# Performance work log

Hardware: AMD Instinct MI355X
Metric: run time of the kernel (lower is better)

## Reference

```python
import jax, jax.numpy as jnp
import numpy as np

NI = 512
HEADS = 8
DH = NI // HEADS  # 64 = attn_chans
EPS = 1e-5

def _ln(x, g, b):
    mu = jnp.mean(x, axis=-1, keepdims=True)
    var = jnp.var(x, axis=-1, keepdims=True)
    return (x - mu) * jax.lax.rsqrt(var + EPS) * g + b

def setup_inputs() -> dict:
    key = jax.random.key(0)
    ks = jax.random.split(key, 5)
    n, c, h, w = 8, NI, 32, 32
    return {
        "x": jax.random.normal(ks[0], (n, c, h, w), jnp.float32),
        "query_x": jax.random.normal(ks[1], (n, c, h, w), jnp.float32),
        "q_ln_g": jnp.ones((c,), jnp.float32),
        "q_ln_b": jnp.zeros((c,), jnp.float32),
        "q_w": jax.random.normal(ks[2], (c, c), jnp.float32) / np.sqrt(c),
        "q_b": jnp.zeros((c,), jnp.float32),
        "kv_ln_g": jnp.ones((c,), jnp.float32),
        "kv_ln_b": jnp.zeros((c,), jnp.float32),
        "kv_w": jax.random.normal(ks[3], (c, 2 * c), jnp.float32) / np.sqrt(c),
        "kv_b": jnp.zeros((2 * c,), jnp.float32),
        "proj_w": jax.random.normal(ks[4], (c, c), jnp.float32) / np.sqrt(c),
        "proj_b": jnp.zeros((c,), jnp.float32),
    }

def reference(x, query_x, q_ln_g, q_ln_b, q_w, q_b, kv_ln_g, kv_ln_b, kv_w, kv_b, proj_w, proj_b):
    n, c, h, w = x.shape
    s = h * w
    xs = x.reshape(n, c, s).transpose(0, 2, 1)        # (n, s, c)
    qx = query_x.reshape(n, c, s).transpose(0, 2, 1)  # (n, s, c)
    q_proj = _ln(qx, q_ln_g, q_ln_b) @ q_w + q_b        # (n, s, c)
    kv = _ln(xs, kv_ln_g, kv_ln_b) @ kv_w + kv_b        # (n, s, 2c)
    cat = jnp.concatenate([q_proj, kv], axis=-1)        # (n, s, 3c)
    # rearrange 'n s (h d3)' with h=HEADS, d3 = 3*DH, then chunk into q,k,v
    cat = cat.reshape(n, s, HEADS, 3 * DH).transpose(0, 2, 1, 3)  # (n, H, s, 3d)
    q, k, v = jnp.split(cat, 3, axis=-1)                # each (n, H, s, d)
    scale = jnp.sqrt(jnp.asarray(DH, q.dtype))          # sqrt(ni/nheads)
    scores = jnp.einsum('nhqd,nhkd->nhqk', q, k) / scale
    attn = jax.nn.softmax(scores, axis=-1)
    o = jnp.einsum('nhqk,nhkd->nhqd', attn, v)          # (n, H, s, d)
    o = o.transpose(0, 2, 1, 3).reshape(n, s, c)        # (n, s, c)
    o = o @ proj_w + proj_b
    return o.transpose(0, 2, 1).reshape(n, c, h, w)
```

## Files before the change

kernel.cpp:

```cpp
#include <hip/hip_runtime.h>
#include <math.h>

namespace {

constexpr int S = 1024;
constexpr int C = 512;
constexpr int NBATCH = 8;
constexpr int RTOT = NBATCH * S;
constexpr int HEADS = 8;
constexpr int DH = 64;

typedef __attribute__((ext_vector_type(8))) short bf16x8;
typedef __attribute__((ext_vector_type(4))) float f32x4;
typedef __attribute__((ext_vector_type(16))) float f32x16;
typedef unsigned short u16;
typedef unsigned int u32;

__device__ __forceinline__ u16 f2bf(float x) {
  union { float f; u32 u; } v; v.f = x;
  u32 r = v.u + 0x7FFF + ((v.u >> 16) & 1);
  return (u16)(r >> 16);
}
__device__ __forceinline__ float bf2f(u16 b) {
  union { u32 u; float f; } v; v.u = (u32)b << 16; return v.f;
}
__device__ __forceinline__ u32 cvtpk(float a, float b) {
  u32 r;
  asm("v_cvt_pk_bf16_f32 %0, %1, %2" : "=v"(r) : "v"(a), "v"(b));
  return r;
}
__device__ __forceinline__ void gl_lds16(const void* g, void* l) {
  auto gp = (const __attribute__((address_space(1))) u32*)g;
  auto lp = (__attribute__((address_space(3))) u32*)l;
  __builtin_amdgcn_global_load_lds(gp, lp, 16, 0, 0);
}

__global__ void ln_fused(const float* __restrict__ x, const float* __restrict__ qx,
                         const float* __restrict__ gx, const float* __restrict__ bx,
                         const float* __restrict__ gq, const float* __restrict__ bq,
                         u16* __restrict__ Xkv, u16* __restrict__ Xq) {
  __shared__ float Ssum[8][32], Ssq[8][32];
  __shared__ float mu_s[32], rs_s[32];
  __shared__ float T[32][65];
  int t = threadIdx.x;
  int si0 = blockIdx.x * 32;
  int isq = blockIdx.y & 1, n = blockIdx.y >> 1;
  const float* in = isq ? qx : x;
  const float* g  = isq ? gq : gx;
  const float* be = isq ? bq : bx;
  u16* out = isq ? Xq : Xkv;

  {
    int sl = t & 31, cg = t >> 5;
    const float* p = in + ((size_t)n * C + cg * 64) * S + si0 + sl;
    float s = 0.f, sq = 0.f;
#pragma unroll 8
    for (int c = 0; c < 64; c++) { float v = p[(size_t)c * S]; s += v; sq += v * v; }
    Ssum[cg][sl] = s; Ssq[cg][sl] = sq;
  }
  __syncthreads();
  if (t < 32) {
    float ss = 0.f, q2 = 0.f;
#pragma unroll
    for (int i = 0; i < 8; i++) { ss += Ssum[i][t]; q2 += Ssq[i][t]; }
    float m = ss * (1.0f / C);
    float var = q2 * (1.0f / C) - m * m;
    mu_s[t] = m; rs_s[t] = rsqrtf(var + 1e-5f);
  }
  __syncthreads();

  int si4 = (t & 7) * 4, cl = t >> 3;
  float4 mu4 = *(const float4*)&mu_s[si4];
  float4 rs4 = *(const float4*)&rs_s[si4];
  int wsl = t >> 3, wc8 = (t & 7) * 8;

  for (int c0 = 0; c0 < C; c0 += 64) {
#pragma unroll
    for (int i = 0; i < 2; i++) {
      int c = c0 + cl + i * 32;
      float4 v = *(const float4*)&in[((size_t)n * C + c) * S + si0 + si4];
      float gg = g[c], bb = be[c];
      T[si4 + 0][cl + i * 32] = (v.x - mu4.x) * rs4.x * gg + bb;
      T[si4 + 1][cl + i * 32] = (v.y - mu4.y) * rs4.y * gg + bb;
      T[si4 + 2][cl + i * 32] = (v.z - mu4.z) * rs4.z * gg + bb;
      T[si4 + 3][cl + i * 32] = (v.w - mu4.w) * rs4.w * gg + bb;
    }
    __syncthreads();
    u16 pk[8];
#pragma unroll
    for (int j = 0; j < 8; j++) pk[j] = f2bf(T[wsl][wc8 + j]);
    *(uint4*)&out[((size_t)(n * S + si0 + wsl)) * C + c0 + wc8] = *(const uint4*)pk;
    __syncthreads();
  }
}

__global__ void prep_w(const float* __restrict__ qw, const float* __restrict__ kvw,
                       const float* __restrict__ pw,
                       u16* __restrict__ Wtq, u16* __restrict__ Wtkv,
                       u16* __restrict__ Wph, u16* __restrict__ Wpl) {
  int z = blockIdx.z;
  int N = (z == 1) ? 1024 : 512;
  int col0 = blockIdx.y * 64;
  if (col0 >= N) return;
  int k0 = blockIdx.x * 64;
  const float* W = (z == 0) ? qw : (z == 1) ? kvw : pw;
  __shared__ float T[64][65];
  int t = threadIdx.x;
  int kl = t >> 4, c4 = (t & 15) * 4;
#pragma unroll
  for (int i = 0; i < 4; i++) {
    float4 v = *(const float4*)&W[(size_t)(k0 + kl + i * 16) * N + col0 + c4];
    T[kl + i * 16][c4 + 0] = v.x; T[kl + i * 16][c4 + 1] = v.y;
    T[kl + i * 16][c4 + 2] = v.z; T[kl + i * 16][c4 + 3] = v.w;
  }
  __syncthreads();
#pragma unroll
  for (int p = 0; p < 2; p++) {
    int cl = (t >> 3) + p * 32, k8 = (t & 7) * 8;
    u16 hi[8], lo[8];
#pragma unroll
    for (int j = 0; j < 8; j++) {
      float f = T[k8 + j][cl];
      u16 hv = f2bf(f);
      hi[j] = hv;
      lo[j] = f2bf(f - bf2f(hv));
    }
    size_t o = (size_t)(col0 + cl) * 512 + k0 + k8;
    if (z == 0) *(uint4*)&Wtq[o] = *(const uint4*)hi;
    else if (z == 1) *(uint4*)&Wtkv[o] = *(const uint4*)hi;
    else { *(uint4*)&Wph[o] = *(const uint4*)hi; *(uint4*)&Wpl[o] = *(const uint4*)lo; }
  }
}

__global__ __launch_bounds__(256, 4) void gemm_qkv(
    const u16* __restrict__ Xq, const u16* __restrict__ Xkv,
    const u16* __restrict__ Wtq, const u16* __restrict__ Wtkv,
    const float* __restrict__ q_b, const float* __restrict__ kv_b,
    u16* __restrict__ Qb, u16* __restrict__ Kb, u16* __restrict__ Vt) {
  __shared__ __attribute__((aligned(16))) u16 As[128 * 64];
  __shared__ __attribute__((aligned(16))) u16 Bs[128 * 64];
  int t = threadIdx.x, wid = t >> 6, lane = t & 63, lr = lane & 15, lg = lane >> 4;
  int colb = blockIdx.x;
  const u16* A; const u16* Wt; const float* bias; int ch0;
  if (colb < 4) { A = Xq;  Wt = Wtq  + (size_t)colb * 128 * 512;       bias = q_b  + colb * 128;       ch0 = colb * 128; }
  else          { A = Xkv; Wt = Wtkv + (size_t)(colb - 4) * 128 * 512; bias = kv_b + (colb - 4) * 128; ch0 = 512 + (colb - 4) * 128; }
  int row0 = blockIdx.y * 128;
  int wr = wid >> 1, wc = wid & 1;
  f32x4 acc[4][4];
#pragma unroll
  for (int m = 0; m < 4; m++)
#pragma unroll
    for (int n = 0; n < 4; n++) acc[m][n] = (f32x4){0.f, 0.f, 0.f, 0.f};

  for (int k0 = 0; k0 < 512; k0 += 64) {
    __syncthreads();
#pragma unroll
    for (int it = 0; it < 4; it++) {
      int chunk = (wid * 4 + it) * 64 + lane;
      int r = chunk >> 3, sg = chunk & 7;
      gl_lds16(A + (size_t)(row0 + r) * 512 + k0 + ((sg ^ (r & 7)) * 8),
               (char*)As + (size_t)chunk * 16);
    }
#pragma unroll
    for (int it = 0; it < 4; it++) {
      int chunk = (wid * 4 + it) * 64 + lane;
      int r = chunk >> 3, sg = chunk & 7;
      gl_lds16(Wt + (size_t)r * 512 + k0 + ((sg ^ (r & 7)) * 8),
               (char*)Bs + (size_t)chunk * 16);
    }
    __syncthreads();
#pragma unroll
    for (int kk = 0; kk < 2; kk++) {
      bf16x8 bfr[4];
#pragma unroll
      for (int n = 0; n < 4; n++) {
        int col = wc * 64 + n * 16 + lr;
        bfr[n] = *(const bf16x8*)((const char*)Bs + col * 128 + (((kk * 4 + lg) ^ (col & 7)) << 4));
      }
#pragma unroll
      for (int m = 0; m < 4; m++) {
        int row = wr * 64 + m * 16 + lr;
        bf16x8 af = *(const bf16x8*)((const char*)As + row * 128 + (((kk * 4 + lg) ^ (row & 7)) << 4));
#pragma unroll
        for (int n = 0; n < 4; n++)
          acc[m][n] = __builtin_amdgcn_mfma_f32_16x16x32_bf16(af, bfr[n], acc[m][n], 0, 0, 0);
      }
    }
  }
#pragma unroll
  for (int m = 0; m < 4; m++)
#pragma unroll
    for (int n = 0; n < 4; n++) {
      int colg = wc * 64 + n * 16 + lr;
      int ch = ch0 + colg;
      int h = ch / 192, role = (ch >> 6) % 3, d = ch & 63;
      float bs = bias[colg];
      float qsc = (role == 0) ? 0.18033688f : 1.0f;
      int growb = row0 + wr * 64 + m * 16 + lg * 4;
      int nn = growb >> 10, ssi0 = growb & (S - 1);
      size_t nh = (size_t)(nn * HEADS + h);
      if (role == 2) {
        u16 pk[4];
#pragma unroll
        for (int r = 0; r < 4; r++) pk[r] = f2bf(acc[m][n][r] + bs);
        *(uint2*)&Vt[(nh * DH + d) * S + ssi0] = *(const uint2*)pk;
      } else {
        u16* dst = (role == 0) ? Qb : Kb;
#pragma unroll
        for (int r = 0; r < 4; r++)
          dst[(nh * S + ssi0 + r) * DH + d] = f2bf((acc[m][n][r] + bs) * qsc);
      }
    }
}

__global__ __launch_bounds__(256) void gemm_proj(
    const u16* __restrict__ Aob, const u16* __restrict__ Wh, const u16* __restrict__ Wl,
    const float* __restrict__ bias, float* __restrict__ out) {
  __shared__ __attribute__((aligned(16))) u16 As[128 * 64];
  __shared__ __attribute__((aligned(16))) u16 Bh[64 * 64];
  __shared__ __attribute__((aligned(16))) u16 Bl[64 * 64];
  int t = threadIdx.x, wid = t >> 6, lane = t & 63, lr = lane & 15, lg = lane >> 4;
  int ch0 = blockIdx.x * 64, row0 = blockIdx.y * 128;
  int wc = wid & 1, wr = wid >> 1;
  f32x4 acc[2][4];
#pragma unroll
  for (int m = 0; m < 2; m++)
#pragma unroll
    for (int n = 0; n < 4; n++) acc[m][n] = (f32x4){0.f, 0.f, 0.f, 0.f};

  for (int k0 = 0; k0 < 512; k0 += 64) {
    __syncthreads();
#pragma unroll
    for (int it = 0; it < 4; it++) {
      int idx = (wid * 4 + it) * 64 + lane;
      int r = idx >> 3, sg = idx & 7;
      gl_lds16(Aob + (size_t)(row0 + r) * 512 + k0 + ((sg ^ (r & 7)) * 8),
               (char*)As + (wid * 4 + it) * 1024);
    }
#pragma unroll
    for (int it = 0; it < 2; it++) {
      int idx = (wid * 2 + it) * 64 + lane;
      int r = idx >> 3, sg = idx & 7;
      size_t go = (size_t)(ch0 + r) * 512 + k0 + ((sg ^ (r & 7)) * 8);
      gl_lds16(Wh + go, (char*)Bh + (wid * 2 + it) * 1024);
      gl_lds16(Wl + go, (char*)Bl + (wid * 2 + it) * 1024);
    }
    __syncthreads();
#pragma unroll
    for (int kk = 0; kk < 2; kk++) {
      bf16x8 ar[4];
#pragma unroll
      for (int n = 0; n < 4; n++) {
        int row = wr * 64 + n * 16 + lr;
        ar[n] = *(const bf16x8*)((const char*)As + row * 128 + (((kk * 4 + lg) ^ (row & 7)) << 4));
      }
#pragma unroll
      for (int m = 0; m < 2; m++) {
        int ch = wc * 32 + m * 16 + lr;
        bf16x8 bh = *(const bf16x8*)((const char*)Bh + ch * 128 + (((kk * 4 + lg) ^ (ch & 7)) << 4));
        bf16x8 bl = *(const bf16x8*)((const char*)Bl + ch * 128 + (((kk * 4 + lg) ^ (ch & 7)) << 4));
#pragma unroll
        for (int n = 0; n < 4; n++) {
          acc[m][n] = __builtin_amdgcn_mfma_f32_16x16x32_bf16(bh, ar[n], acc[m][n], 0, 0, 0);
          acc[m][n] = __builtin_amdgcn_mfma_f32_16x16x32_bf16(bl, ar[n], acc[m][n], 0, 0, 0);
        }
      }
    }
  }
#pragma unroll
  for (int m = 0; m < 2; m++)
#pragma unroll
    for (int n = 0; n < 4; n++) {
      int rowg = row0 + wr * 64 + n * 16 + lr;
      int nn = rowg >> 10, ssi = rowg & (S - 1);
#pragma unroll
      for (int r = 0; r < 4; r++) {
        int ch = ch0 + wc * 32 + m * 16 + lg * 4 + r;
        out[((size_t)nn * C + ch) * S + ssi] = acc[m][n][r] + bias[ch];
      }
    }
}

constexpr int KVB = 64;

__global__ __launch_bounds__(256) void attn_kernel(
    const u16* __restrict__ Qbf, const u16* __restrict__ Kbf,
    const u16* __restrict__ Vtb, u16* __restrict__ Obf) {
  __shared__ __attribute__((aligned(16))) u16 Ks[2][KVB * DH];
  __shared__ __attribute__((aligned(16))) u16 Vs[2][DH * KVB];

  int tid = threadIdx.x;
  int wave = tid >> 6, lane = tid & 63;
  int lq = lane & 31, hi = lane >> 5;
  int w = (blockIdx.x & 7) * 64 + (blockIdx.x >> 3);
  int qt = w & 7, nh = w >> 3;
  const u16* Qg = Qbf + (size_t)nh * S * DH;
  const u16* Kg = Kbf + (size_t)nh * S * DH;
  const u16* Vg = Vtb + (size_t)nh * DH * S;

  int qrow = qt * 128 + wave * 32 + lq;
  bf16x8 qf[4];
#pragma unroll
  for (int ks = 0; ks < 4; ks++)
    qf[ks] = *(const bf16x8*)(Qg + (size_t)qrow * DH + ks * 16 + hi * 8);

  f32x16 oa0 = {}, oa1 = {};
  float m_run = -1e30f, l_run = 0.f;

  int e0i = tid, e1i = tid + 256;
  int r0 = e0i >> 3, sg0 = e0i & 7, r1 = e1i >> 3, sg1 = e1i & 7;
  char* kd0 = (char*)&Ks[0][0] + (e0i & ~63) * 16;
  char* kd1 = (char*)&Ks[0][0] + (e1i & ~63) * 16;
  char* vd0 = (char*)&Vs[0][0] + (e0i & ~63) * 16;
  char* vd1 = (char*)&Vs[0][0] + (e1i & ~63) * 16;

#define STAGE(kb, b)                                                             \
  do {                                                                           \
    gl_lds16(Kg + (size_t)((kb) * KVB + r0) * 64 + ((sg0 ^ (r0 & 7)) * 8),       \
             kd0 + (b) * (KVB * DH * 2));                                        \
    gl_lds16(Kg + (size_t)((kb) * KVB + r1) * 64 + ((sg1 ^ (r1 & 7)) * 8),       \
             kd1 + (b) * (KVB * DH * 2));                                        \
    gl_lds16(Vg + (size_t)r0 * S + (kb) * KVB + ((sg0 ^ (r0 & 7)) * 8),          \
             vd0 + (b) * (KVB * DH * 2));                                        \
    gl_lds16(Vg + (size_t)r1 * S + (kb) * KVB + ((sg1 ^ (r1 & 7)) * 8),          \
             vd1 + (b) * (KVB * DH * 2));                                        \
  } while (0)

  STAGE(0, 0);

  for (int kb = 0; kb < S / KVB; kb++) {
    int cur = kb & 1;
    __syncthreads();
    if (kb + 1 < S / KVB) STAGE(kb + 1, cur ^ 1);

    const char* Kc = (const char*)&Ks[cur][0];
    const char* Vc = (const char*)&Vs[cur][0];

    f32x16 sc0 = {}, sc1 = {};
#pragma unroll
    for (int ks = 0; ks < 4; ks++) {
      int row0k = lq;
      int row1k = 32 + lq;
      int sg = ks * 2 + hi;
      bf16x8 kf0 = *(const bf16x8*)(Kc + row0k * 128 + ((sg ^ (lq & 7)) << 4));
      bf16x8 kf1 = *(const bf16x8*)(Kc + row1k * 128 + ((sg ^ (lq & 7)) << 4));
      sc0 = __builtin_amdgcn_mfma_f32_32x32x16_bf16(kf0, qf[ks], sc0, 0, 0, 0);
      sc1 = __builtin_amdgcn_mfma_f32_32x32x16_bf16(kf1, qf[ks], sc1, 0, 0, 0);
    }

    float pmax = -1e30f;
#pragma unroll
    for (int r = 0; r < 16; r++) pmax = fmaxf(pmax, fmaxf(sc0[r], sc1[r]));
    pmax = fmaxf(pmax, __shfl_xor(pmax, 32));

    if (!__all(pmax <= m_run + 11.5f)) {
      float mnew = fmaxf(m_run, pmax);
      float corr = exp2f(m_run - mnew);
      m_run = mnew;
      l_run *= corr;
#pragma unroll
      for (int r = 0; r < 16; r++) { oa0[r] *= corr; oa1[r] *= corr; }
    }

    float psum = 0.f;
#pragma unroll
    for (int r = 0; r < 16; r++) { sc0[r] = exp2f(sc0[r] - m_run); psum += sc0[r]; }
#pragma unroll
    for (int r = 0; r < 16; r++) { sc1[r] = exp2f(sc1[r] - m_run); psum += sc1[r]; }
    psum += __shfl_xor(psum, 32);
    l_run += psum;

    u32 c[16];
    c[0]  = cvtpk(sc0[0],  sc0[1]);  c[1]  = cvtpk(sc0[2],  sc0[3]);
    c[2]  = cvtpk(sc0[4],  sc0[5]);  c[3]  = cvtpk(sc0[6],  sc0[7]);
    c[4]  = cvtpk(sc0[8],  sc0[9]);  c[5]  = cvtpk(sc0[10], sc0[11]);
    c[6]  = cvtpk(sc0[12], sc0[13]); c[7]  = cvtpk(sc0[14], sc0[15]);
    c[8]  = cvtpk(sc1[0],  sc1[1]);  c[9]  = cvtpk(sc1[2],  sc1[3]);
    c[10] = cvtpk(sc1[4],  sc1[5]);  c[11] = cvtpk(sc1[6],  sc1[7]);
    c[12] = cvtpk(sc1[8],  sc1[9]);  c[13] = cvtpk(sc1[10], sc1[11]);
    c[14] = cvtpk(sc1[12], sc1[13]); c[15] = cvtpk(sc1[14], sc1[15]);
    asm("v_permlane32_swap_b32 %0, %1" : "+v"(c[0]),  "+v"(c[2]));
    asm("v_permlane32_swap_b32 %0, %1" : "+v"(c[1]),  "+v"(c[3]));
    asm("v_permlane32_swap_b32 %0, %1" : "+v"(c[4]),  "+v"(c[6]));
    asm("v_permlane32_swap_b32 %0, %1" : "+v"(c[5]),  "+v"(c[7]));
    asm("v_permlane32_swap_b32 %0, %1" : "+v"(c[8]),  "+v"(c[10]));
    asm("v_permlane32_swap_b32 %0, %1" : "+v"(c[9]),  "+v"(c[11]));
    asm("v_permlane32_swap_b32 %0, %1" : "+v"(c[12]), "+v"(c[14]));
    asm("v_permlane32_swap_b32 %0, %1" : "+v"(c[13]), "+v"(c[15]));

#pragma unroll
    for (int kk = 0; kk < 4; kk++) {
      union { u32 u[4]; bf16x8 v; } pu;
      pu.u[0] = c[kk * 4 + 0]; pu.u[1] = c[kk * 4 + 1];
      pu.u[2] = c[kk * 4 + 2]; pu.u[3] = c[kk * 4 + 3];
      int sg = kk * 2 + hi;
      bf16x8 vf0 = *(const bf16x8*)(Vc + lq * 128 + ((sg ^ (lq & 7)) << 4));
      bf16x8 vf1 = *(const bf16x8*)(Vc + (32 + lq) * 128 + ((sg ^ (lq & 7)) << 4));
      oa0 = __builtin_amdgcn_mfma_f32_32x32x16_bf16(vf0, pu.v, oa0, 0, 0, 0);
      oa1 = __builtin_amdgcn_mfma_f32_32x32x16_bf16(vf1, pu.v, oa1, 0, 0, 0);
    }
  }
#undef STAGE

  int n = nh >> 3, h = nh & 7;
  float lf = 1.0f / l_run;
  u16* orow = Obf + ((size_t)n * S + qrow) * C + h * DH;
#pragma unroll
  for (int rq = 0; rq < 4; rq++) {
    int d0 = rq * 8 + 4 * hi;
    uint2 w0, w1;
    w0.x = cvtpk(oa0[rq * 4 + 0] * lf, oa0[rq * 4 + 1] * lf);
    w0.y = cvtpk(oa0[rq * 4 + 2] * lf, oa0[rq * 4 + 3] * lf);
    w1.x = cvtpk(oa1[rq * 4 + 0] * lf, oa1[rq * 4 + 1] * lf);
    w1.y = cvtpk(oa1[rq * 4 + 2] * lf, oa1[rq * 4 + 3] * lf);
    *(uint2*)(orow + d0) = w0;
    *(uint2*)(orow + 32 + d0) = w1;
  }
}

}

extern "C" void kernel_launch(void* const* d_in, const int* in_sizes, int n_in,
                              void* d_out, int out_size, void* d_ws, size_t ws_size,
                              hipStream_t stream) {
  const float* x       = (const float*)d_in[0];
  const float* qx      = (const float*)d_in[1];
  const float* q_ln_g  = (const float*)d_in[2];
  const float* q_ln_b  = (const float*)d_in[3];
  const float* q_w     = (const float*)d_in[4];
  const float* q_b     = (const float*)d_in[5];
  const float* kv_ln_g = (const float*)d_in[6];
  const float* kv_ln_b = (const float*)d_in[7];
  const float* kv_w    = (const float*)d_in[8];
  const float* kv_b    = (const float*)d_in[9];
  const float* proj_w  = (const float*)d_in[10];
  const float* proj_b  = (const float*)d_in[11];
  float* out = (float*)d_out;

  u16* u = (u16*)d_ws;
  u16* Xkv  = u;                u += (size_t)RTOT * C;
  u16* Xq   = u;                u += (size_t)RTOT * C;
  u16* Wtq  = u;                u += (size_t)C * C;
  u16* Wtkv = u;                u += (size_t)2 * C * C;
  u16* Wph  = u;                u += (size_t)C * C;
  u16* Wpl  = u;                u += (size_t)C * C;
  u16* Qb   = u;                u += (size_t)NBATCH * HEADS * S * DH;
  u16* Kb   = u;                u += (size_t)NBATCH * HEADS * S * DH;
  u16* Vt   = u;                u += (size_t)NBATCH * HEADS * S * DH;
  u16* Obf  = u;

  hipLaunchKernelGGL(ln_fused, dim3(S / 32, 2 * NBATCH), dim3(256), 0, stream,
                     x, qx, kv_ln_g, kv_ln_b, q_ln_g, q_ln_b, Xkv, Xq);
  hipLaunchKernelGGL(prep_w, dim3(8, 16, 3), dim3(256), 0, stream,
                     q_w, kv_w, proj_w, Wtq, Wtkv, Wph, Wpl);
  hipLaunchKernelGGL(gemm_qkv, dim3(12, RTOT / 128), dim3(256), 0, stream,
                     Xq, Xkv, Wtq, Wtkv, q_b, kv_b, Qb, Kb, Vt);
  hipLaunchKernelGGL(attn_kernel, dim3(512), dim3(256), 0, stream,
                     Qb, Kb, Vt, Obf);
  hipLaunchKernelGGL(gemm_proj, dim3(C / 64, RTOT / 128), dim3(256), 0, stream,
                     Obf, Wph, Wpl, proj_b, out);
}
```

Measured before the change: 98.53 us.

## Split attention KV range across wave pairs and merge partial softmax via LDS

Each attention block now covers 64 query rows instead of 128, with two wave groups each handling half of every 64-key tile. The partial max, sum and output accumulators are combined through shared memory at the end, and the grid doubles to 1024 blocks. This is meant to raise parallelism and occupancy (launch bounds now request 4 blocks per unit) on a grid that previously had only 512 blocks. In exchange, K/V tiles are loaded once per 64 queries rather than per 128, which doubles LDS staging traffic, and an LDS merge with extra barriers is added.

New measurement: 95.73 us. -2.8%, faster.

```diff
diff --git a/kernel.cpp b/kernel.cpp
--- a/kernel.cpp
+++ b/kernel.cpp
@@ -283,7 +283,7 @@
 
 constexpr int KVB = 64;
 
-__global__ __launch_bounds__(256) void attn_kernel(
+__global__ __launch_bounds__(256, 4) void attn_kernel(
     const u16* __restrict__ Qbf, const u16* __restrict__ Kbf,
     const u16* __restrict__ Vtb, u16* __restrict__ Obf) {
   __shared__ __attribute__((aligned(16))) u16 Ks[2][KVB * DH];
@@ -292,13 +292,14 @@
   int tid = threadIdx.x;
   int wave = tid >> 6, lane = tid & 63;
   int lq = lane & 31, hi = lane >> 5;
-  int w = (blockIdx.x & 7) * 64 + (blockIdx.x >> 3);
-  int qt = w & 7, nh = w >> 3;
+  int qg = wave & 1, kg = wave >> 1;
+  int w = (blockIdx.x & 7) * 128 + (blockIdx.x >> 3);
+  int qt = w & 15, nh = w >> 4;
   const u16* Qg = Qbf + (size_t)nh * S * DH;
   const u16* Kg = Kbf + (size_t)nh * S * DH;
   const u16* Vg = Vtb + (size_t)nh * DH * S;
 
-  int qrow = qt * 128 + wave * 32 + lq;
+  int qrow = qt * 64 + qg * 32 + lq;
   bf16x8 qf[4];
 #pragma unroll
   for (int ks = 0; ks < 4; ks++)
@@ -336,21 +337,20 @@
     const char* Kc = (const char*)&Ks[cur][0];
     const char* Vc = (const char*)&Vs[cur][0];
 
-    f32x16 sc0 = {}, sc1 = {};
+    f32x16 sc = {};
 #pragma unroll
     for (int ks = 0; ks < 4; ks++) {
-      int row0k = lq;
-      int row1k = 32 + lq;
       int sg = ks * 2 + hi;
-      bf16x8 kf0 = *(const bf16x8*)(Kc + row0k * 128 + ((sg ^ (lq & 7)) << 4));
-      bf16x8 kf1 = *(const bf16x8*)(Kc + row1k * 128 + ((sg ^ (lq & 7)) << 4));
-      sc0 = __builtin_amdgcn_mfma_f32_32x32x16_bf16(kf0, qf[ks], sc0, 0, 0, 0);
-      sc1 = __builtin_amdgcn_mfma_f32_32x32x16_bf16(kf1, qf[ks], sc1, 0, 0, 0);
-    }
-
-    float pmax = -1e30f;
-#pragma unroll
-    for (int r = 0; r < 16; r++) pmax = fmaxf(pmax, fmaxf(sc0[r], sc1[r]));
+      bf16x8 kf = *(const bf16x8*)(Kc + (kg * 32 + lq) * 128 + ((sg ^ (lq & 7)) << 4));
+      sc = __builtin_amdgcn_mfma_f32_32x32x16_bf16(kf, qf[ks], sc, 0, 0, 0);
+    }
+
+    float mx[8];
+#pragma unroll
+    for (int r = 0; r < 8; r++) mx[r] = fmaxf(sc[2 * r], sc[2 * r + 1]);
+#pragma unroll
+    for (int r = 0; r < 4; r++) mx[r] = fmaxf(mx[r], mx[r + 4]);
+    float pmax = fmaxf(fmaxf(mx[0], mx[1]), fmaxf(mx[2], mx[3]));
     pmax = fmaxf(pmax, __shfl_xor(pmax, 32));
 
     if (!__all(pmax <= m_run + 11.5f)) {
@@ -362,38 +362,35 @@
       for (int r = 0; r < 16; r++) { oa0[r] *= corr; oa1[r] *= corr; }
     }
 
-    float psum = 0.f;
-#pragma unroll
-    for (int r = 0; r < 16; r++) { sc0[r] = exp2f(sc0[r] - m_run); psum += sc0[r]; }
-#pragma unroll
-    for (int r = 0; r < 16; r++) { sc1[r] = exp2f(sc1[r] - m_run); psum += sc1[r]; }
-    psum += __shfl_xor(psum, 32);
-    l_run += psum;
-
-    u32 c[16];
-    c[0]  = cvtpk(sc0[0],  sc0[1]);  c[1]  = cvtpk(sc0[2],  sc0[3]);
-    c[2]  = cvtpk(sc0[4],  sc0[5]);  c[3]  = cvtpk(sc0[6],  sc0[7]);
-    c[4]  = cvtpk(sc0[8],  sc0[9]);  c[5]  = cvtpk(sc0[10], sc0[11]);
-    c[6]  = cvtpk(sc0[12], sc0[13]); c[7]  = cvtpk(sc0[14], sc0[15]);
-    c[8]  = cvtpk(sc1[0],  sc1[1]);  c[9]  = cvtpk(sc1[2],  sc1[3]);
-    c[10] = cvtpk(sc1[4],  sc1[5]);  c[11] = cvtpk(sc1[6],  sc1[7]);
-    c[12] = cvtpk(sc1[8],  sc1[9]);  c[13] = cvtpk(sc1[10], sc1[11]);
-    c[14] = cvtpk(sc1[12], sc1[13]); c[15] = cvtpk(sc1[14], sc1[15]);
-    asm("v_permlane32_swap_b32 %0, %1" : "+v"(c[0]),  "+v"(c[2]));
-    asm("v_permlane32_swap_b32 %0, %1" : "+v"(c[1]),  "+v"(c[3]));
-    asm("v_permlane32_swap_b32 %0, %1" : "+v"(c[4]),  "+v"(c[6]));
-    asm("v_permlane32_swap_b32 %0, %1" : "+v"(c[5]),  "+v"(c[7]));
-    asm("v_permlane32_swap_b32 %0, %1" : "+v"(c[8]),  "+v"(c[10]));
-    asm("v_permlane32_swap_b32 %0, %1" : "+v"(c[9]),  "+v"(c[11]));
-    asm("v_permlane32_swap_b32 %0, %1" : "+v"(c[12]), "+v"(c[14]));
-    asm("v_permlane32_swap_b32 %0, %1" : "+v"(c[13]), "+v"(c[15]));
-
-#pragma unroll
-    for (int kk = 0; kk < 4; kk++) {
+#pragma unroll
+    for (int r = 0; r < 16; r++) sc[r] = exp2f(sc[r] - m_run);
+    {
+      float s8[8];
+#pragma unroll
+      for (int r = 0; r < 8; r++) s8[r] = sc[2 * r] + sc[2 * r + 1];
+#pragma unroll
+      for (int r = 0; r < 4; r++) s8[r] += s8[r + 4];
+      float psum = (s8[0] + s8[1]) + (s8[2] + s8[3]);
+      psum += __shfl_xor(psum, 32);
+      l_run += psum;
+    }
+
+    u32 c[8];
+    c[0] = cvtpk(sc[0],  sc[1]);  c[1] = cvtpk(sc[2],  sc[3]);
+    c[2] = cvtpk(sc[4],  sc[5]);  c[3] = cvtpk(sc[6],  sc[7]);
+    c[4] = cvtpk(sc[8],  sc[9]);  c[5] = cvtpk(sc[10], sc[11]);
+    c[6] = cvtpk(sc[12], sc[13]); c[7] = cvtpk(sc[14], sc[15]);
+    asm("v_permlane32_swap_b32 %0, %1" : "+v"(c[0]), "+v"(c[2]));
+    asm("v_permlane32_swap_b32 %0, %1" : "+v"(c[1]), "+v"(c[3]));
+    asm("v_permlane32_swap_b32 %0, %1" : "+v"(c[4]), "+v"(c[6]));
+    asm("v_permlane32_swap_b32 %0, %1" : "+v"(c[5]), "+v"(c[7]));
+
+#pragma unroll
+    for (int kk = 0; kk < 2; kk++) {
       union { u32 u[4]; bf16x8 v; } pu;
       pu.u[0] = c[kk * 4 + 0]; pu.u[1] = c[kk * 4 + 1];
       pu.u[2] = c[kk * 4 + 2]; pu.u[3] = c[kk * 4 + 3];
-      int sg = kk * 2 + hi;
+      int sg = kg * 4 + kk * 2 + hi;
       bf16x8 vf0 = *(const bf16x8*)(Vc + lq * 128 + ((sg ^ (lq & 7)) << 4));
       bf16x8 vf1 = *(const bf16x8*)(Vc + (32 + lq) * 128 + ((sg ^ (lq & 7)) << 4));
       oa0 = __builtin_amdgcn_mfma_f32_32x32x16_bf16(vf0, pu.v, oa0, 0, 0, 0);
@@ -402,19 +399,46 @@
   }
 #undef STAGE
 
-  int n = nh >> 3, h = nh & 7;
-  float lf = 1.0f / l_run;
-  u16* orow = Obf + ((size_t)n * S + qrow) * C + h * DH;
-#pragma unroll
-  for (int rq = 0; rq < 4; rq++) {
-    int d0 = rq * 8 + 4 * hi;
-    uint2 w0, w1;
-    w0.x = cvtpk(oa0[rq * 4 + 0] * lf, oa0[rq * 4 + 1] * lf);
-    w0.y = cvtpk(oa0[rq * 4 + 2] * lf, oa0[rq * 4 + 3] * lf);
-    w1.x = cvtpk(oa1[rq * 4 + 0] * lf, oa1[rq * 4 + 1] * lf);
-    w1.y = cvtpk(oa1[rq * 4 + 2] * lf, oa1[rq * 4 + 3] * lf);
-    *(uint2*)(orow + d0) = w0;
-    *(uint2*)(orow + 32 + d0) = w1;
+  __syncthreads();
+  float* exO = (float*)&Ks[0][0];
+  float* exS = (float*)&Vs[0][0];
+  if (kg) {
+    float* o = exO + qg * 2048;
+#pragma unroll
+    for (int r = 0; r < 16; r++) {
+      o[r * 64 + lane] = oa0[r];
+      o[(16 + r) * 64 + lane] = oa1[r];
+    }
+    exS[qg * 128 + lane] = m_run;
+    exS[qg * 128 + 64 + lane] = l_run;
+  }
+  __syncthreads();
+  if (!kg) {
+    float* o = exO + qg * 2048;
+    float m2 = exS[qg * 128 + lane];
+    float l2 = exS[qg * 128 + 64 + lane];
+    float m = fmaxf(m_run, m2);
+    float f0 = exp2f(m_run - m), f2 = exp2f(m2 - m);
+    l_run = l_run * f0 + l2 * f2;
+#pragma unroll
+    for (int r = 0; r < 16; r++) {
+      oa0[r] = oa0[r] * f0 + o[r * 64 + lane] * f2;
+      oa1[r] = oa1[r] * f0 + o[(16 + r) * 64 + lane] * f2;
+    }
+    int n = nh >> 3, h = nh & 7;
+    float lf = 1.0f / l_run;
+    u16* orow = Obf + ((size_t)n * S + qrow) * C + h * DH;
+#pragma unroll
+    for (int rq = 0; rq < 4; rq++) {
+      int d0 = rq * 8 + 4 * hi;
+      uint2 w0, w1;
+      w0.x = cvtpk(oa0[rq * 4 + 0] * lf, oa0[rq * 4 + 1] * lf);
+      w0.y = cvtpk(oa0[rq * 4 + 2] * lf, oa0[rq * 4 + 3] * lf);
+      w1.x = cvtpk(oa1[rq * 4 + 0] * lf, oa1[rq * 4 + 1] * lf);
+      w1.y = cvtpk(oa1[rq * 4 + 2] * lf, oa1[rq * 4 + 3] * lf);
+      *(uint2*)(orow + d0) = w0;
+      *(uint2*)(orow + 32 + d0) = w1;
+    }
   }
 }
 
@@ -455,7 +479,7 @@
                      q_w, kv_w, proj_w, Wtq, Wtkv, Wph, Wpl);
   hipLaunchKernelGGL(gemm_qkv, dim3(12, RTOT / 128), dim3(256), 0, stream,
                      Xq, Xkv, Wtq, Wtkv, q_b, kv_b, Qb, Kb, Vt);
-  hipLaunchKernelGGL(attn_kernel, dim3(512), dim3(256), 0, stream,
+  hipLaunchKernelGGL(attn_kernel, dim3(1024), dim3(256), 0, stream,
                      Qb, Kb, Vt, Obf);
   hipLaunchKernelGGL(gemm_proj, dim3(C / 64, RTOT / 128), dim3(256), 0, stream,
                      Obf, Wph, Wpl, proj_b, out);
```
